# Performance work log

Hardware: AMD Instinct MI355X
Metric: run time of the kernel (lower is better)

## Reference

```python
import jax, jax.numpy as jnp
import numpy as np

N, M, D = 32768, 4096, 128  # samples, SOM units (64x64), input_dim
GRID_H, GRID_W = 64, 64


def setup_inputs() -> dict:
    key = jax.random.key(0)
    k1, k2 = jax.random.split(key)
    inputs = jax.random.normal(k1, (N, D), dtype=jnp.float32)
    # SOM2D.__init__: weights = torch.rand(size, input_dim)
    weights = jax.random.uniform(k2, (M, D), dtype=jnp.float32)
    # grid = meshgrid(arange(H), arange(W)) -> [M, 2] integer unit coordinates
    gx, gy = jnp.meshgrid(jnp.arange(GRID_H), jnp.arange(GRID_W), indexing='ij')
    grid = jnp.stack([gx, gy], axis=-1).reshape(-1, 2).astype(jnp.int32)
    return {"inputs": inputs, "weights": weights, "grid": grid}


def reference(inputs, weights, grid):
    # sed(x, y): squared Euclidean distance [N, M].
    # tensor the torch code materializes; same math.
    x_sq = jnp.sum(inputs * inputs, axis=1, keepdims=True)        # [N, 1]
    w_sq = jnp.sum(weights * weights, axis=1)                      # [M]
    cross = jnp.einsum('nd,md->nm', inputs, weights)               # [N, M]
    distances = x_sq + w_sq - 2.0 * cross                          # [N, M]
    # wtac: argmin over units, then lookup grid coordinates of the winner.
    winning_indices = jnp.argmin(distances, axis=1)                # [N]
    winning_labels = grid[winning_indices]                         # [N, 2]
    return winning_labels
```

## Files before the change

kernel.cpp:

```cpp
#include <hip/hip_runtime.h>
#include <float.h>
#include <stdint.h>


constexpr int D = 128;

typedef _Float16 f16x8 __attribute__((ext_vector_type(8)));
typedef float    f32x4 __attribute__((ext_vector_type(4)));

__device__ __forceinline__ void cvt_split(const float4& a0, const float4& a1,
                                          f16x8& h, f16x8& l) {
    float v[8] = {a0.x, a0.y, a0.z, a0.w, a1.x, a1.y, a1.z, a1.w};
#pragma unroll
    for (int j = 0; j < 8; ++j) {
        _Float16 hh = (_Float16)v[j];
        h[j] = hh;
        l[j] = (_Float16)(v[j] - (float)hh);
    }
}

__global__ __launch_bounds__(256) void prep_kernel(
        const float* __restrict__ w, f16x8* __restrict__ hG,
        f16x8* __restrict__ lG, float* __restrict__ wsq, int M,
        unsigned long long* __restrict__ keys, unsigned* __restrict__ cnt,
        int N, int nGroups) {
    int g = blockIdx.x * 256 + threadIdx.x;
    if (keys && g < N) keys[g] = ~0ull;
    if (cnt && g < nGroups) cnt[g] = 0u;
    if (g >= M * 16) return;
    int u = g >> 4, o = g & 15;
    const float4* wp = reinterpret_cast<const float4*>(w + (size_t)u * D + o * 8);
    float4 a0 = wp[0], a1 = wp[1];
    f16x8 h, l;
    cvt_split(a0, a1, h, l);
    float ss = 0.f;
    ss = fmaf(a0.x, a0.x, ss); ss = fmaf(a0.y, a0.y, ss);
    ss = fmaf(a0.z, a0.z, ss); ss = fmaf(a0.w, a0.w, ss);
    ss = fmaf(a1.x, a1.x, ss); ss = fmaf(a1.y, a1.y, ss);
    ss = fmaf(a1.z, a1.z, ss); ss = fmaf(a1.w, a1.w, ss);
#pragma unroll
    for (int m = 1; m < 16; m <<= 1) ss += __shfl_xor(ss, m, 64);
    if (o == 0) wsq[u] = ss;
    int slot = ((u >> 5) << 9) + ((o >> 2) << 7) + (((u >> 4) & 1) << 6)
             + ((o & 3) << 4) + (u & 15);
    hG[slot] = h;
    lG[slot] = l;
}

template <bool PARTIAL>
__global__ __launch_bounds__(256, 2) void som_main(
        const float* __restrict__ x, const f16x8* __restrict__ hG,
        const f16x8* __restrict__ lG, const float* __restrict__ wsq,
        const int* __restrict__ grid, int* __restrict__ out,
        unsigned long long* __restrict__ keys, unsigned* __restrict__ cnt,
        int unitGroups, int tilesQ, int tilesR, int N) {
    __shared__ f16x8 albuf[4 * 1024];
    __shared__ int lastFlag;

    const int tid  = threadIdx.x;
    const int lane = tid & 63;
    const int wv   = tid >> 6;
    const int c    = lane & 15;
    const int q    = lane >> 4;

    const int ug    = blockIdx.x % unitGroups;
    const int sg    = blockIdx.x / unitGroups;
    const int sWave = sg * 256 + wv * 64;

    f16x8* myAl = &albuf[wv * 1024];

    f16x8 Ah[16];
#pragma unroll
    for (int i = 0; i < 4; ++i) {
        const float* xr = x + (size_t)(sWave + 16 * i + c) * D + q * 8;
#pragma unroll
        for (int s = 0; s < 4; ++s) {
            float4 a0 = *reinterpret_cast<const float4*>(xr + 32 * s);
            float4 a1 = *reinterpret_cast<const float4*>(xr + 32 * s + 4);
            f16x8 h, l;
            cvt_split(a0, a1, h, l);
            Ah[i * 4 + s] = h;
            myAl[(i * 4 + s) * 64 + lane] = l;
        }
    }

    float bestD[16];
    int   bestI[16];
#pragma unroll
    for (int sl = 0; sl < 16; ++sl) { bestD[sl] = FLT_MAX; bestI[sl] = 0; }

    const int tile0  = ug * tilesQ + (ug < tilesR ? ug : tilesR);
    const int tcount = tilesQ + (ug < tilesR ? 1 : 0);

    f16x8 bh[8], bl[8];
    {
        const f16x8* hp = hG + ((size_t)tile0 << 9) + lane;
        const f16x8* lp = lG + ((size_t)tile0 << 9) + lane;
#pragma unroll
        for (int s = 0; s < 4; ++s)
#pragma unroll
            for (int t = 0; t < 2; ++t) {
                bh[s * 2 + t] = hp[s * 128 + t * 64];
                bl[s * 2 + t] = lp[s * 128 + t * 64];
            }
    }

    for (int tt = 0; tt < tcount; ++tt) {
        const int tile  = tile0 + tt;
        const int uTile = tile * 32;
        const float wq0 = wsq[uTile + c];
        const float wq1 = wsq[uTile + 16 + c];

        const int nxt = (tt + 1 < tcount) ? (tile + 1) : tile0;
        const f16x8* hp = hG + ((size_t)nxt << 9) + lane;
        const f16x8* lp = lG + ((size_t)nxt << 9) + lane;

        f32x4 acc[8];
#pragma unroll
        for (int f = 0; f < 8; ++f) acc[f] = (f32x4){0.f, 0.f, 0.f, 0.f};

        __builtin_amdgcn_s_setprio(1);
#pragma unroll
        for (int s = 0; s < 4; ++s)
#pragma unroll
            for (int i = 0; i < 4; ++i)
#pragma unroll
                for (int t = 0; t < 2; ++t)
                    acc[i * 2 + t] = __builtin_amdgcn_mfma_f32_16x16x32_f16(
                        Ah[i * 4 + s], bh[s * 2 + t], acc[i * 2 + t], 0, 0, 0);
#pragma unroll
        for (int s = 0; s < 4; ++s) {
            f16x8 al[4];
#pragma unroll
            for (int i = 0; i < 4; ++i) al[i] = myAl[(i * 4 + s) * 64 + lane];
#pragma unroll
            for (int i = 0; i < 4; ++i)
#pragma unroll
                for (int t = 0; t < 2; ++t)
                    acc[i * 2 + t] = __builtin_amdgcn_mfma_f32_16x16x32_f16(
                        al[i], bh[s * 2 + t], acc[i * 2 + t], 0, 0, 0);
        }
        __builtin_amdgcn_s_setprio(0);

#pragma unroll
        for (int s = 0; s < 4; ++s)
#pragma unroll
            for (int t = 0; t < 2; ++t)
                bh[s * 2 + t] = hp[s * 128 + t * 64];

        __builtin_amdgcn_s_setprio(1);
#pragma unroll
        for (int s = 0; s < 4; ++s)
#pragma unroll
            for (int i = 0; i < 4; ++i)
#pragma unroll
                for (int t = 0; t < 2; ++t)
                    acc[i * 2 + t] = __builtin_amdgcn_mfma_f32_16x16x32_f16(
                        Ah[i * 4 + s], bl[s * 2 + t], acc[i * 2 + t], 0, 0, 0);
        __builtin_amdgcn_s_setprio(0);

#pragma unroll
        for (int s = 0; s < 4; ++s)
#pragma unroll
            for (int t = 0; t < 2; ++t)
                bl[s * 2 + t] = lp[s * 128 + t * 64];

#pragma unroll
        for (int t = 0; t < 2; ++t) {
            const int n    = uTile + 16 * t + c;
            const float wq = t == 0 ? wq0 : wq1;
#pragma unroll
            for (int i = 0; i < 4; ++i) {
                f32x4 a = acc[i * 2 + t];
#pragma unroll
                for (int r = 0; r < 4; ++r) {
                    float score = fmaf(-2.f, a[r], wq);
                    int sl = i * 4 + r;
                    if (score < bestD[sl]) { bestD[sl] = score; bestI[sl] = n; }
                }
            }
        }
    }

#pragma unroll
    for (int sl = 0; sl < 16; ++sl) {
        float d   = bestD[sl];
        int   idx = bestI[sl];
#pragma unroll
        for (int m = 1; m < 16; m <<= 1) {
            float od = __shfl_xor(d, m, 64);
            int   oi = __shfl_xor(idx, m, 64);
            if (od < d || (od == d && oi < idx)) { d = od; idx = oi; }
        }
        if (c == 0) {
            const int sOut = sWave + 16 * (sl >> 2) + 4 * q + (sl & 3);
            if (PARTIAL) {
                unsigned ub = __float_as_uint(d);
                ub = (ub & 0x80000000u) ? ~ub : (ub | 0x80000000u);
                unsigned long long key = ((unsigned long long)ub << 32) | (unsigned)idx;
                atomicMin(&keys[sOut], key);
            } else {
                out[2 * sOut]     = grid[2 * idx];
                out[2 * sOut + 1] = grid[2 * idx + 1];
            }
        }
    }

    if (PARTIAL) {
        __threadfence();
        __syncthreads();
        if (tid == 0)
            lastFlag = (atomicAdd(&cnt[sg], 1u) == (unsigned)(unitGroups - 1));
        __syncthreads();
        if (lastFlag) {
            const int s0 = sg * 256 + tid;
            unsigned long long k = atomicMin(&keys[s0], ~0ull);
            int idx = (int)(unsigned)(k & 0xFFFFFFFFull);
            out[2 * s0]     = grid[2 * idx];
            out[2 * s0 + 1] = grid[2 * idx + 1];
        }
    }
}

extern "C" void kernel_launch(void* const* d_in, const int* in_sizes, int n_in,
                              void* d_out, int out_size, void* d_ws, size_t ws_size,
                              hipStream_t stream) {
    const float* x    = (const float*)d_in[0];
    const float* w    = (const float*)d_in[1];
    const int*   grid = (const int*)d_in[2];
    int* out = (int*)d_out;

    const int N = in_sizes[0] / D;
    const int M = in_sizes[1] / D;

    const size_t hlBytes   = (size_t)M * D * 2;
    const size_t baseBytes = 2 * hlBytes + (size_t)M * 4;
    const int sampleGroups = N / 256;
    const size_t needBytes = baseBytes + (size_t)N * 8 + (size_t)sampleGroups * 4;

    f16x8* hG  = (f16x8*)d_ws;
    f16x8* lG  = (f16x8*)((char*)d_ws + hlBytes);
    float* wsq = (float*)((char*)d_ws + 2 * hlBytes);
    unsigned long long* keys = (unsigned long long*)((char*)d_ws + baseBytes);
    unsigned* cnt = (unsigned*)((char*)d_ws + baseBytes + (size_t)N * 8);

    const int tiles = M / 32;
    const int UG = (ws_size >= needBytes) ? 4 : 1;

    prep_kernel<<<(M * 16 + 255) / 256, 256, 0, stream>>>(
        w, hG, lG, wsq, M,
        UG > 1 ? keys : nullptr, UG > 1 ? cnt : nullptr, N, sampleGroups);

    const int tq = tiles / UG, trm = tiles % UG;
    if (UG > 1) {
        som_main<true><<<sampleGroups * UG, 256, 0, stream>>>(
            x, hG, lG, wsq, grid, out, keys, cnt, UG, tq, trm, N);
    } else {
        som_main<false><<<sampleGroups, 256, 0, stream>>>(
            x, hG, lG, wsq, grid, out, nullptr, nullptr, 1, tiles, 0, N);
    }
}
```

Baseline: 180.9 us.

## Double-buffer MFMA accumulators and fold wsq into accumulator init

Restructures the tile loop so each step computes the current tile into one accumulator set while the argmin scoring of the previous tile runs interleaved between MFMA phases, using two ping-pong accumulator arrays. The accumulator is initialized with -0.5*||w||^2 so the score becomes a max over x·w - 0.5||w||^2, removing the per-element fma, and the final value is rescaled by -2. B-fragment loads are now issued at the start of each step rather than prefetched a tile ahead, and the setprio hints are dropped. Doubling the accumulators raises register pressure, which may hurt occupancy at the 2-blocks launch bound.

```diff
diff --git a/kernel.cpp b/kernel.cpp
--- a/kernel.cpp
+++ b/kernel.cpp
@@ -47,6 +47,85 @@
     lG[slot] = l;
 }
 
+__device__ __forceinline__ void score_block(
+        const f32x4 (&acc)[8], int tile, int c,
+        float (&bestD)[16], int (&bestI)[16]) {
+    const int uTile = tile * 32;
+#pragma unroll
+    for (int t = 0; t < 2; ++t) {
+        const int n = uTile + 16 * t + c;
+#pragma unroll
+        for (int i = 0; i < 4; ++i) {
+            f32x4 a = acc[i * 2 + t];
+#pragma unroll
+            for (int r = 0; r < 4; ++r) {
+                int sl = i * 4 + r;
+                if (a[r] > bestD[sl]) { bestD[sl] = a[r]; bestI[sl] = n; }
+            }
+        }
+    }
+}
+
+template <bool SCORE_PREV>
+__device__ __forceinline__ void tile_step(
+        const f16x8 (&Ah)[16], const f16x8* myAl, int lane, int c,
+        const f16x8* __restrict__ hG, const f16x8* __restrict__ lG,
+        const float* __restrict__ wsq, int tile,
+        f32x4 (&cur)[8], const f32x4 (&prev)[8], int prevTile,
+        float (&bestD)[16], int (&bestI)[16]) {
+    const f16x8* hp = hG + ((size_t)tile << 9) + lane;
+    const f16x8* lp = lG + ((size_t)tile << 9) + lane;
+    f16x8 bh[8], bl[8];
+#pragma unroll
+    for (int s = 0; s < 4; ++s)
+#pragma unroll
+        for (int t = 0; t < 2; ++t) {
+            bh[s * 2 + t] = hp[s * 128 + t * 64];
+            bl[s * 2 + t] = lp[s * 128 + t * 64];
+        }
+
+    const int uTile = tile * 32;
+    const float m0 = -0.5f * wsq[uTile + c];
+    const float m1 = -0.5f * wsq[uTile + 16 + c];
+#pragma unroll
+    for (int i = 0; i < 4; ++i) {
+        cur[i * 2 + 0] = (f32x4){m0, m0, m0, m0};
+        cur[i * 2 + 1] = (f32x4){m1, m1, m1, m1};
+    }
+
+#pragma unroll
+    for (int s = 0; s < 4; ++s)
+#pragma unroll
+        for (int i = 0; i < 4; ++i)
+#pragma unroll
+            for (int t = 0; t < 2; ++t)
+                cur[i * 2 + t] = __builtin_amdgcn_mfma_f32_16x16x32_f16(
+                    Ah[i * 4 + s], bh[s * 2 + t], cur[i * 2 + t], 0, 0, 0);
+#pragma unroll
+    for (int s = 0; s < 4; ++s) {
+        f16x8 al[4];
+#pragma unroll
+        for (int i = 0; i < 4; ++i) al[i] = myAl[(i * 4 + s) * 64 + lane];
+#pragma unroll
+        for (int i = 0; i < 4; ++i)
+#pragma unroll
+            for (int t = 0; t < 2; ++t)
+                cur[i * 2 + t] = __builtin_amdgcn_mfma_f32_16x16x32_f16(
+                    al[i], bh[s * 2 + t], cur[i * 2 + t], 0, 0, 0);
+    }
+
+    if (SCORE_PREV) score_block(prev, prevTile, c, bestD, bestI);
+
+#pragma unroll
+    for (int s = 0; s < 4; ++s)
+#pragma unroll
+        for (int i = 0; i < 4; ++i)
+#pragma unroll
+            for (int t = 0; t < 2; ++t)
+                cur[i * 2 + t] = __builtin_amdgcn_mfma_f32_16x16x32_f16(
+                    Ah[i * 4 + s], bl[s * 2 + t], cur[i * 2 + t], 0, 0, 0);
+}
+
 template <bool PARTIAL>
 __global__ __launch_bounds__(256, 2) void som_main(
         const float* __restrict__ x, const f16x8* __restrict__ hG,
@@ -87,104 +166,33 @@
     float bestD[16];
     int   bestI[16];
 #pragma unroll
-    for (int sl = 0; sl < 16; ++sl) { bestD[sl] = FLT_MAX; bestI[sl] = 0; }
+    for (int sl = 0; sl < 16; ++sl) { bestD[sl] = -FLT_MAX; bestI[sl] = 0; }
 
     const int tile0  = ug * tilesQ + (ug < tilesR ? ug : tilesR);
     const int tcount = tilesQ + (ug < tilesR ? 1 : 0);
 
-    f16x8 bh[8], bl[8];
-    {
-        const f16x8* hp = hG + ((size_t)tile0 << 9) + lane;
-        const f16x8* lp = lG + ((size_t)tile0 << 9) + lane;
-#pragma unroll
-        for (int s = 0; s < 4; ++s)
-#pragma unroll
-            for (int t = 0; t < 2; ++t) {
-                bh[s * 2 + t] = hp[s * 128 + t * 64];
-                bl[s * 2 + t] = lp[s * 128 + t * 64];
-            }
-    }
-
-    for (int tt = 0; tt < tcount; ++tt) {
-        const int tile  = tile0 + tt;
-        const int uTile = tile * 32;
-        const float wq0 = wsq[uTile + c];
-        const float wq1 = wsq[uTile + 16 + c];
-
-        const int nxt = (tt + 1 < tcount) ? (tile + 1) : tile0;
-        const f16x8* hp = hG + ((size_t)nxt << 9) + lane;
-        const f16x8* lp = lG + ((size_t)nxt << 9) + lane;
-
-        f32x4 acc[8];
-#pragma unroll
-        for (int f = 0; f < 8; ++f) acc[f] = (f32x4){0.f, 0.f, 0.f, 0.f};
-
-        __builtin_amdgcn_s_setprio(1);
-#pragma unroll
-        for (int s = 0; s < 4; ++s)
-#pragma unroll
-            for (int i = 0; i < 4; ++i)
-#pragma unroll
-                for (int t = 0; t < 2; ++t)
-                    acc[i * 2 + t] = __builtin_amdgcn_mfma_f32_16x16x32_f16(
-                        Ah[i * 4 + s], bh[s * 2 + t], acc[i * 2 + t], 0, 0, 0);
-#pragma unroll
-        for (int s = 0; s < 4; ++s) {
-            f16x8 al[4];
-#pragma unroll
-            for (int i = 0; i < 4; ++i) al[i] = myAl[(i * 4 + s) * 64 + lane];
-#pragma unroll
-            for (int i = 0; i < 4; ++i)
-#pragma unroll
-                for (int t = 0; t < 2; ++t)
-                    acc[i * 2 + t] = __builtin_amdgcn_mfma_f32_16x16x32_f16(
-                        al[i], bh[s * 2 + t], acc[i * 2 + t], 0, 0, 0);
-        }
-        __builtin_amdgcn_s_setprio(0);
-
-#pragma unroll
-        for (int s = 0; s < 4; ++s)
-#pragma unroll
-            for (int t = 0; t < 2; ++t)
-                bh[s * 2 + t] = hp[s * 128 + t * 64];
-
-        __builtin_amdgcn_s_setprio(1);
-#pragma unroll
-        for (int s = 0; s < 4; ++s)
-#pragma unroll
-            for (int i = 0; i < 4; ++i)
-#pragma unroll
-                for (int t = 0; t < 2; ++t)
-                    acc[i * 2 + t] = __builtin_amdgcn_mfma_f32_16x16x32_f16(
-                        Ah[i * 4 + s], bl[s * 2 + t], acc[i * 2 + t], 0, 0, 0);
-        __builtin_amdgcn_s_setprio(0);
-
-#pragma unroll
-        for (int s = 0; s < 4; ++s)
-#pragma unroll
-            for (int t = 0; t < 2; ++t)
-                bl[s * 2 + t] = lp[s * 128 + t * 64];
-
-#pragma unroll
-        for (int t = 0; t < 2; ++t) {
-            const int n    = uTile + 16 * t + c;
-            const float wq = t == 0 ? wq0 : wq1;
-#pragma unroll
-            for (int i = 0; i < 4; ++i) {
-                f32x4 a = acc[i * 2 + t];
-#pragma unroll
-                for (int r = 0; r < 4; ++r) {
-                    float score = fmaf(-2.f, a[r], wq);
-                    int sl = i * 4 + r;
-                    if (score < bestD[sl]) { bestD[sl] = score; bestI[sl] = n; }
-                }
-            }
-        }
+    f32x4 accA[8], accB[8];
+
+    tile_step<false>(Ah, myAl, lane, c, hG, lG, wsq, tile0,
+                     accA, accB, 0, bestD, bestI);
+    int tt = 1;
+    for (; tt + 1 < tcount; tt += 2) {
+        tile_step<true>(Ah, myAl, lane, c, hG, lG, wsq, tile0 + tt,
+                        accB, accA, tile0 + tt - 1, bestD, bestI);
+        tile_step<true>(Ah, myAl, lane, c, hG, lG, wsq, tile0 + tt + 1,
+                        accA, accB, tile0 + tt, bestD, bestI);
+    }
+    if (tt < tcount) {
+        tile_step<true>(Ah, myAl, lane, c, hG, lG, wsq, tile0 + tt,
+                        accB, accA, tile0 + tt - 1, bestD, bestI);
+        score_block(accB, tile0 + tt, c, bestD, bestI);
+    } else {
+        score_block(accA, tile0 + tcount - 1, c, bestD, bestI);
     }
 
 #pragma unroll
     for (int sl = 0; sl < 16; ++sl) {
-        float d   = bestD[sl];
+        float d   = -2.0f * bestD[sl];
         int   idx = bestI[sl];
 #pragma unroll
         for (int m = 1; m < 16; m <<= 1) {
```

New measurement: 260.2 us. +43.8%, slower.
